# Kernel optimization log

Hardware: AMD Instinct MI355X
Metric: run time of the kernel (lower is better)

## Reference

```python
import jax, jax.numpy as jnp
import numpy as np

N, IN_DIM, OUT_DIM, HEADS, E = 50000, 256, 256, 4, 800000
HEAD_DIM = OUT_DIM // HEADS
NEG_SLOPE = 0.2


def setup_inputs() -> dict:
    key = jax.random.key(0)
    k = jax.random.split(key, 6)
    h = jax.random.normal(k[0], (N, IN_DIM), dtype=jnp.float32)
    edge_index = jax.random.randint(k[1], (2, E), 0, N, dtype=jnp.int32)
    # xavier-uniform-ish scales
    W = jax.random.normal(k[2], (OUT_DIM, IN_DIM), dtype=jnp.float32) * (1.0 / np.sqrt(IN_DIM))
    b = jnp.zeros((OUT_DIM,), dtype=jnp.float32)
    a_src = jax.random.normal(k[3], (HEADS, HEAD_DIM), dtype=jnp.float32) * (1.0 / np.sqrt(HEAD_DIM))
    a_dst = jax.random.normal(k[4], (HEADS, HEAD_DIM), dtype=jnp.float32) * (1.0 / np.sqrt(HEAD_DIM))
    return {"h": h, "edge_index": edge_index, "W": W, "b": b, "a_src": a_src, "a_dst": a_dst}


def reference(h, edge_index, W, b, a_src, a_dst):
    idx_i, idx_j = edge_index[0], edge_index[1]
    Wh = (h @ W.T + b).reshape(N, HEADS, HEAD_DIM)  # [N,H,D]
    # per-node attention logits components (avoids gathering full Wh per edge twice)
    alpha_src = jnp.einsum('nhd,hd->nh', Wh, a_src)  # [N,H]
    alpha_dst = jnp.einsum('nhd,hd->nh', Wh, a_dst)  # [N,H]
    e = jax.nn.leaky_relu(alpha_src[idx_i] + alpha_dst[idx_j], NEG_SLOPE)  # [E,H]
    # segment softmax over neighbors j of each destination row i (sparse.softmax dim=1)
    m = jax.ops.segment_max(e, idx_i, num_segments=N)  # [N,H]
    ex = jnp.exp(e - m[idx_i])
    denom = jax.ops.segment_sum(ex, idx_i, num_segments=N)  # [N,H]
    att = ex / denom[idx_i]  # [E,H]
    # sparse-mm aggregation: out_i = sum_j att_ij * Wh_j, per head
    out = jax.ops.segment_sum(att[:, :, None] * Wh[idx_j], idx_i, num_segments=N)  # [N,H,D]
    return out.reshape(N, OUT_DIM)
```

## Files before the change

### kernel.cpp

```cpp
#include <hip/hip_runtime.h>
#include <hip/hip_bf16.h>
#include <stdint.h>

constexpr int IN_DIM  = 256;
constexpr int OUT_DIM = 256;
constexpr int HEADS   = 4;
constexpr int HEAD_DIM = 64;
constexpr float NEG_SLOPE = 0.2f;

typedef __attribute__((ext_vector_type(8))) short bf16x8;
typedef __attribute__((ext_vector_type(4))) float f32x4;

static __device__ __forceinline__ unsigned short f2bf(float f) {
  union { float f; uint32_t u; } v; v.f = f;
  uint32_t u = v.u;
  return (unsigned short)((u + 0x7fffu + ((u >> 16) & 1u)) >> 16);
}

__global__ __launch_bounds__(256) void k_prep(
    const float* __restrict__ W, const float* __restrict__ b,
    const float* __restrict__ a_src, const float* __restrict__ a_dst,
    float* __restrict__ csrc, unsigned short* __restrict__ Wb) {
  int bid = blockIdx.x, t = threadIdx.x;
  if (bid < 32) {
    int base = bid * 2048 + t * 8;
    float4 f0 = *(const float4*)(W + base);
    float4 f1 = *(const float4*)(W + base + 4);
    union { unsigned short us[8]; uint4 u4; } pk;
    pk.us[0]=f2bf(f0.x); pk.us[1]=f2bf(f0.y); pk.us[2]=f2bf(f0.z); pk.us[3]=f2bf(f0.w);
    pk.us[4]=f2bf(f1.x); pk.us[5]=f2bf(f1.y); pk.us[6]=f2bf(f1.z); pk.us[7]=f2bf(f1.w);
    *(uint4*)(Wb + base) = pk.u4;
  } else if (t < 8) {
    int hh = t & 3;
    const float* a = (t < 4 ? a_src : a_dst) + hh * HEAD_DIM;
    float cs = 0.f;
    for (int d = 0; d < HEAD_DIM; ++d) cs += b[hh * HEAD_DIM + d] * a[d];
    csrc[t] = cs;
  }
}

__global__ __launch_bounds__(256) void k_gemm_mfma(
    const float* __restrict__ h, const unsigned short* __restrict__ Wb,
    const float* __restrict__ b,
    const float* __restrict__ a_src, const float* __restrict__ a_dst,
    const float* __restrict__ csrc,
    unsigned short* __restrict__ Wh,
    float* __restrict__ asrc, float* __restrict__ adst,
    const int* __restrict__ idx_i, int* __restrict__ counts, int N, int E) {
  __shared__ unsigned short lds[20480];
  const int t = threadIdx.x;
  const int w = t >> 6, l = t & 63;
  const int lm = l & 15, g = l >> 4;
  const int r0 = blockIdx.x * 64;

  f32x4 acc[4][4];
  const f32x4 fz = {0.f, 0.f, 0.f, 0.f};
#pragma unroll
  for (int fm = 0; fm < 4; ++fm)
#pragma unroll
    for (int fn = 0; fn < 4; ++fn) acc[fm][fn] = fz;

  float breg[4], asg[4], adg[4];
#pragma unroll
  for (int fn = 0; fn < 4; ++fn) {
    breg[fn] = b[w * 64 + fn * 16 + lm];
    asg[fn]  = a_src[w * 64 + fn * 16 + lm];
    adg[fn]  = a_dst[w * 64 + fn * 16 + lm];
  }

  auto stageA = [&](int ch) {
    int k0 = ch * 64;
    int row = t >> 2;
    int grow = r0 + row;
    unsigned short* dstbase = lds + row * 64;
#pragma unroll
    for (int cc = 0; cc < 2; ++cc) {
      int c = (t & 3) * 2 + cc;
      union { unsigned short us[8]; bf16x8 v; } pk;
      if (grow < N) {
        const float* src = h + (size_t)grow * 256 + k0 + c * 8;
        float4 f0 = *(const float4*)(src);
        float4 f1 = *(const float4*)(src + 4);
        pk.us[0]=f2bf(f0.x); pk.us[1]=f2bf(f0.y); pk.us[2]=f2bf(f0.z); pk.us[3]=f2bf(f0.w);
        pk.us[4]=f2bf(f1.x); pk.us[5]=f2bf(f1.y); pk.us[6]=f2bf(f1.z); pk.us[7]=f2bf(f1.w);
      } else {
#pragma unroll
        for (int e = 0; e < 8; ++e) pk.us[e] = 0;
      }
      *(bf16x8*)(dstbase + ((c ^ (row & 7)) * 8)) = pk.v;
    }
  };

  auto stageB = [&](int ch) {
    int k0 = ch * 64;
    unsigned short* Bbase = lds + 4096;
    int c  = l & 7;
    int rs = l >> 3;
#pragma unroll
    for (int i = 0; i < 8; ++i) {
      int row = w * 64 + i * 8 + rs;
      bf16x8 v = *(const bf16x8*)(Wb + (size_t)row * 256 + k0 + c * 8);
      *(bf16x8*)(Bbase + row * 64 + ((c ^ rs) * 8)) = v;
    }
  };

  auto compute = [&]() {
    const unsigned short* A = lds;
    const unsigned short* B = lds + 4096;
#pragma unroll
    for (int ks = 0; ks < 2; ++ks) {
      bf16x8 af[4], bfr[4];
#pragma unroll
      for (int fm = 0; fm < 4; ++fm) {
        int row = fm * 16 + lm;
        af[fm] = *(const bf16x8*)(A + row * 64 + (((ks * 4 + g) ^ (row & 7)) * 8));
      }
#pragma unroll
      for (int fn = 0; fn < 4; ++fn) {
        int row = w * 64 + fn * 16 + lm;
        bfr[fn] = *(const bf16x8*)(B + row * 64 + (((ks * 4 + g) ^ (row & 7)) * 8));
      }
#pragma unroll
      for (int fm = 0; fm < 4; ++fm)
#pragma unroll
        for (int fn = 0; fn < 4; ++fn)
          acc[fm][fn] = __builtin_amdgcn_mfma_f32_16x16x32_bf16(
              af[fm], bfr[fn], acc[fm][fn], 0, 0, 0);
    }
  };

#pragma unroll
  for (int ch = 0; ch < 4; ++ch) {
    stageA(ch); stageB(ch);
    __syncthreads();
    compute();
    __syncthreads();
  }

#pragma unroll
  for (int fm = 0; fm < 4; ++fm) {
#pragma unroll
    for (int r = 0; r < 4; ++r) {
      int grow = r0 + fm * 16 + g * 4 + r;
      if (grow < N) {
        size_t rowoff = (size_t)grow * 256;
#pragma unroll
        for (int fn = 0; fn < 4; ++fn) {
          int col = w * 64 + fn * 16 + lm;
          Wh[rowoff + col] = f2bf(acc[fm][fn][r] + breg[fn]);
        }
      }
    }
  }

  float cs = csrc[w], cd = csrc[4 + w];
#pragma unroll
  for (int fm = 0; fm < 4; ++fm) {
#pragma unroll
    for (int r = 0; r < 4; ++r) {
      float ps = acc[fm][0][r] * asg[0] + acc[fm][1][r] * asg[1]
               + acc[fm][2][r] * asg[2] + acc[fm][3][r] * asg[3];
      float pd = acc[fm][0][r] * adg[0] + acc[fm][1][r] * adg[1]
               + acc[fm][2][r] * adg[2] + acc[fm][3][r] * adg[3];
#pragma unroll
      for (int off = 1; off < 16; off <<= 1) {
        ps += __shfl_xor(ps, off, 64);
        pd += __shfl_xor(pd, off, 64);
      }
      if (lm == 0) {
        int grow = r0 + fm * 16 + g * 4 + r;
        if (grow < N) {
          asrc[grow * 4 + w] = ps + cs;
          adst[grow * 4 + w] = pd + cd;
        }
      }
    }
  }

  {
    long long nb = gridDim.x;
    long long e0 = (long long)blockIdx.x * E / nb;
    long long e1 = ((long long)blockIdx.x + 1) * E / nb;
    for (long long e = e0 + t; e < e1; e += 256)
      atomicAdd(&counts[idx_i[e]], 1);
  }
}

__global__ __launch_bounds__(256) void k_scanA(const int* __restrict__ counts,
                                               int* __restrict__ offsets,
                                               int* __restrict__ bsum, int N) {
  __shared__ int s[256];
  int t = threadIdx.x;
  int idx = blockIdx.x * 256 + t;
  int v = (idx < N) ? counts[idx] : 0;
  s[t] = v;
  __syncthreads();
  for (int off = 1; off < 256; off <<= 1) {
    int x = (t >= off) ? s[t - off] : 0;
    __syncthreads();
    s[t] += x;
    __syncthreads();
  }
  if (idx < N) offsets[idx] = s[t] - v;
  if (t == 255) bsum[blockIdx.x] = s[255];
}

__global__ __launch_bounds__(256) void k_scanBC(int* __restrict__ offsets,
                                                const int* __restrict__ bsum,
                                                int nb, int N) {
  __shared__ int s[256];
  int t = threadIdx.x;
  int v = (t < nb) ? bsum[t] : 0;
  s[t] = v;
  __syncthreads();
  for (int off = 1; off < 256; off <<= 1) {
    int x = (t >= off) ? s[t - off] : 0;
    __syncthreads();
    s[t] += x;
    __syncthreads();
  }
  int bid = blockIdx.x;
  int add = (bid > 0) ? s[bid - 1] : 0;
  int idx = bid * 256 + t;
  if (idx < N) offsets[idx] += add;
}

__global__ __launch_bounds__(256) void k_scatter(const int* __restrict__ idx_i,
                                                 const int* __restrict__ idx_j,
                                                 int* __restrict__ offsets,
                                                 int* __restrict__ csr_j, int E) {
  int e = blockIdx.x * 256 + threadIdx.x;
  if (e < E) {
    int i = idx_i[e];
    int p = atomicAdd(&offsets[i], 1);
    csr_j[p] = idx_j[e];
  }
}

__global__ __launch_bounds__(256) void k_aggregate(const int* __restrict__ offsets,
                                                   const int* __restrict__ csr_j,
                                                   const float* __restrict__ asrc,
                                                   const float* __restrict__ adst,
                                                   const unsigned short* __restrict__ Wh,
                                                   float* __restrict__ out, int N) {
  int t = threadIdx.x;
  int wv = t >> 6, l = t & 63;
  int half = l >> 5, ll = l & 31;
  int i = blockIdx.x * 8 + wv * 2 + half;
  bool valid = i < N;
  int beg = (valid && i > 0) ? offsets[i - 1] : 0;
  int end = valid ? offsets[i] : 0;
  int deg = end - beg;
  int hh = ll >> 3;
  float aih = valid ? asrc[i * 4 + hh] : 0.f;

  float o[8];
#pragma unroll
  for (int d = 0; d < 8; ++d) o[d] = 0.f;
  float denom = 0.f;

  for (int q = 0; q < deg; q += 8) {
    int jj[8];
    float wgt[8];
    uint4 vv[8];
#pragma unroll
    for (int k = 0; k < 8; ++k) {
      int qk = q + k;
      int qc = qk < deg - 1 ? qk : deg - 1;
      jj[k] = csr_j[beg + qc];
    }
#pragma unroll
    for (int k = 0; k < 8; ++k) {
      float s = aih + adst[(size_t)jj[k] * 4 + hh];
      s = s > 0.f ? s : NEG_SLOPE * s;
      s = (q + k < deg) ? s : -1e38f;
      wgt[k] = __expf(s);
      vv[k] = *(const uint4*)(Wh + (size_t)jj[k] * 256 + ll * 8);
    }
    denom += ((wgt[0] + wgt[1]) + (wgt[2] + wgt[3])) +
             ((wgt[4] + wgt[5]) + (wgt[6] + wgt[7]));
#pragma unroll
    for (int k = 0; k < 8; ++k) {
      union { uint32_t u; float f; } c0, c1, c2, c3, c4, c5, c6, c7;
      c0.u = vv[k].x << 16; c1.u = vv[k].x & 0xffff0000u;
      c2.u = vv[k].y << 16; c3.u = vv[k].y & 0xffff0000u;
      c4.u = vv[k].z << 16; c5.u = vv[k].z & 0xffff0000u;
      c6.u = vv[k].w << 16; c7.u = vv[k].w & 0xffff0000u;
      float wk = wgt[k];
      o[0] += wk * c0.f; o[1] += wk * c1.f;
      o[2] += wk * c2.f; o[3] += wk * c3.f;
      o[4] += wk * c4.f; o[5] += wk * c5.f;
      o[6] += wk * c6.f; o[7] += wk * c7.f;
    }
  }

  if (valid) {
    float inv = (deg > 0) ? 1.f / denom : 0.f;
    f32x4 o0 = {o[0] * inv, o[1] * inv, o[2] * inv, o[3] * inv};
    f32x4 o1 = {o[4] * inv, o[5] * inv, o[6] * inv, o[7] * inv};
    f32x4* dst = (f32x4*)(out + (size_t)i * 256 + ll * 8);
    __builtin_nontemporal_store(o0, dst);
    __builtin_nontemporal_store(o1, dst + 1);
  }
}

extern "C" void kernel_launch(void* const* d_in, const int* in_sizes, int n_in,
                              void* d_out, int out_size, void* d_ws, size_t ws_size,
                              hipStream_t stream) {
  const float* h     = (const float*)d_in[0];
  const int*   eidx  = (const int*)  d_in[1];
  const float* W     = (const float*)d_in[2];
  const float* b     = (const float*)d_in[3];
  const float* a_src = (const float*)d_in[4];
  const float* a_dst = (const float*)d_in[5];
  float* out = (float*)d_out;

  const int N = in_sizes[0] / IN_DIM;
  const int E = in_sizes[1] / 2;
  const int* idx_i = eidx;
  const int* idx_j = eidx + E;

  char* p = (char*)d_ws;
  auto alloc = [&](size_t bytes) {
    char* r = p;
    p += (bytes + 255) & ~(size_t)255;
    return r;
  };
  float* csrc = (float*)alloc(8 * sizeof(float));
  unsigned short* Wb = (unsigned short*)alloc((size_t)OUT_DIM * IN_DIM * sizeof(unsigned short));
  unsigned short* Wh = (unsigned short*)alloc((size_t)N * OUT_DIM * sizeof(unsigned short));
  float* asrc = (float*)alloc((size_t)N * HEADS * sizeof(float));
  float* adst = (float*)alloc((size_t)N * HEADS * sizeof(float));
  int* counts  = (int*)alloc((size_t)N * sizeof(int));
  int* offsets = (int*)alloc(((size_t)N + 1) * sizeof(int));
  int* bsum    = (int*)alloc(256 * sizeof(int));
  int* csrj    = (int*)alloc((size_t)E * sizeof(int));

  const int nbN = (N + 255) / 256;
  const int nbE = (E + 255) / 256;
  const int nbM = (N + 63) / 64;

  (void)hipMemsetAsync(counts, 0, (size_t)N * sizeof(int), stream);
  k_prep<<<33, 256, 0, stream>>>(W, b, a_src, a_dst, csrc, Wb);
  k_gemm_mfma<<<nbM, 256, 0, stream>>>(h, Wb, b, a_src, a_dst, csrc,
                                       Wh, asrc, adst, idx_i, counts, N, E);
  k_scanA<<<nbN, 256, 0, stream>>>(counts, offsets, bsum, N);
  k_scanBC<<<nbN, 256, 0, stream>>>(offsets, bsum, nbN, N);
  k_scatter<<<nbE, 256, 0, stream>>>(idx_i, idx_j, offsets, csrj, E);
  k_aggregate<<<(N + 7) / 8, 256, 0, stream>>>(offsets, csrj, asrc, adst, Wh, out, N);
}
```

Measured before the change: 187.8 us.

## Load GEMM operands directly to registers, fold memset into prep, widen scan

The GEMM drops LDS staging and loads h (fp32) and bf16 W fragments from global memory straight into registers. It converts them with v_cvt_pk_bf16_f32 and double-buffers the register loads across eight k-steps, with no barriers. The counts memset is folded into k_prep, saving one launch. The scan kernels now process four elements per thread, cutting the block count. Global loads become uncoalesced per-lane row reads, and the same operands are re-read by multiple waves, relying on cache instead of LDS reuse.

```diff
diff --git a/kernel.cpp b/kernel.cpp
--- a/kernel.cpp
+++ b/kernel.cpp
@@ -17,11 +17,20 @@
   return (unsigned short)((u + 0x7fffu + ((u >> 16) & 1u)) >> 16);
 }
 
+static __device__ __forceinline__ uint32_t cvt_pk(float lo, float hi) {
+  uint32_t r;
+  asm("v_cvt_pk_bf16_f32 %0, %1, %2" : "=v"(r) : "v"(lo), "v"(hi));
+  return r;
+}
+
 __global__ __launch_bounds__(256) void k_prep(
     const float* __restrict__ W, const float* __restrict__ b,
     const float* __restrict__ a_src, const float* __restrict__ a_dst,
-    float* __restrict__ csrc, unsigned short* __restrict__ Wb) {
+    float* __restrict__ csrc, unsigned short* __restrict__ Wb,
+    int* __restrict__ counts, int N) {
   int bid = blockIdx.x, t = threadIdx.x;
+  int i = bid * 256 + t;
+  if (i < N) counts[i] = 0;
   if (bid < 32) {
     int base = bid * 2048 + t * 8;
     float4 f0 = *(const float4*)(W + base);
@@ -30,7 +39,7 @@
     pk.us[0]=f2bf(f0.x); pk.us[1]=f2bf(f0.y); pk.us[2]=f2bf(f0.z); pk.us[3]=f2bf(f0.w);
     pk.us[4]=f2bf(f1.x); pk.us[5]=f2bf(f1.y); pk.us[6]=f2bf(f1.z); pk.us[7]=f2bf(f1.w);
     *(uint4*)(Wb + base) = pk.u4;
-  } else if (t < 8) {
+  } else if (bid == 32 && t < 8) {
     int hh = t & 3;
     const float* a = (t < 4 ? a_src : a_dst) + hh * HEAD_DIM;
     float cs = 0.f;
@@ -47,12 +56,21 @@
     unsigned short* __restrict__ Wh,
     float* __restrict__ asrc, float* __restrict__ adst,
     const int* __restrict__ idx_i, int* __restrict__ counts, int N, int E) {
-  __shared__ unsigned short lds[20480];
   const int t = threadIdx.x;
   const int w = t >> 6, l = t & 63;
   const int lm = l & 15, g = l >> 4;
   const int r0 = blockIdx.x * 64;
 
+  const float* aptr[4];
+  const unsigned short* bptr[4];
+#pragma unroll
+  for (int f = 0; f < 4; ++f) {
+    int grow = r0 + f * 16 + lm;
+    if (grow > N - 1) grow = N - 1;
+    aptr[f] = h + (size_t)grow * 256 + g * 8;
+    bptr[f] = Wb + (size_t)(w * 64 + f * 16 + lm) * 256 + g * 8;
+  }
+
   f32x4 acc[4][4];
   const f32x4 fz = {0.f, 0.f, 0.f, 0.f};
 #pragma unroll
@@ -68,73 +86,45 @@
     adg[fn]  = a_dst[w * 64 + fn * 16 + lm];
   }
 
-  auto stageA = [&](int ch) {
-    int k0 = ch * 64;
-    int row = t >> 2;
-    int grow = r0 + row;
-    unsigned short* dstbase = lds + row * 64;
-#pragma unroll
-    for (int cc = 0; cc < 2; ++cc) {
-      int c = (t & 3) * 2 + cc;
-      union { unsigned short us[8]; bf16x8 v; } pk;
-      if (grow < N) {
-        const float* src = h + (size_t)grow * 256 + k0 + c * 8;
-        float4 f0 = *(const float4*)(src);
-        float4 f1 = *(const float4*)(src + 4);
-        pk.us[0]=f2bf(f0.x); pk.us[1]=f2bf(f0.y); pk.us[2]=f2bf(f0.z); pk.us[3]=f2bf(f0.w);
-        pk.us[4]=f2bf(f1.x); pk.us[5]=f2bf(f1.y); pk.us[6]=f2bf(f1.z); pk.us[7]=f2bf(f1.w);
-      } else {
-#pragma unroll
-        for (int e = 0; e < 8; ++e) pk.us[e] = 0;
-      }
-      *(bf16x8*)(dstbase + ((c ^ (row & 7)) * 8)) = pk.v;
+  f32x4 aA[4][2], aB[4][2];
+  bf16x8 bA[4], bB[4];
+
+  auto load_step = [&](int s, f32x4 (&A)[4][2], bf16x8 (&B)[4]) {
+    int off = s * 32;
+#pragma unroll
+    for (int f = 0; f < 4; ++f) {
+      A[f][0] = *(const f32x4*)(aptr[f] + off);
+      A[f][1] = *(const f32x4*)(aptr[f] + off + 4);
+      B[f] = *(const bf16x8*)(bptr[f] + off);
     }
   };
 
-  auto stageB = [&](int ch) {
-    int k0 = ch * 64;
-    unsigned short* Bbase = lds + 4096;
-    int c  = l & 7;
-    int rs = l >> 3;
-#pragma unroll
-    for (int i = 0; i < 8; ++i) {
-      int row = w * 64 + i * 8 + rs;
-      bf16x8 v = *(const bf16x8*)(Wb + (size_t)row * 256 + k0 + c * 8);
-      *(bf16x8*)(Bbase + row * 64 + ((c ^ rs) * 8)) = v;
-    }
+  auto compute_step = [&](f32x4 (&A)[4][2], bf16x8 (&B)[4]) {
+    bf16x8 af[4];
+#pragma unroll
+    for (int f = 0; f < 4; ++f) {
+      union { uint32_t u[4]; bf16x8 v; } pk;
+      pk.u[0] = cvt_pk(A[f][0].x, A[f][0].y);
+      pk.u[1] = cvt_pk(A[f][0].z, A[f][0].w);
+      pk.u[2] = cvt_pk(A[f][1].x, A[f][1].y);
+      pk.u[3] = cvt_pk(A[f][1].z, A[f][1].w);
+      af[f] = pk.v;
+    }
+#pragma unroll
+    for (int fm = 0; fm < 4; ++fm)
+#pragma unroll
+      for (int fn = 0; fn < 4; ++fn)
+        acc[fm][fn] = __builtin_amdgcn_mfma_f32_16x16x32_bf16(
+            af[fm], B[fn], acc[fm][fn], 0, 0, 0);
   };
 
-  auto compute = [&]() {
-    const unsigned short* A = lds;
-    const unsigned short* B = lds + 4096;
-#pragma unroll
-    for (int ks = 0; ks < 2; ++ks) {
-      bf16x8 af[4], bfr[4];
-#pragma unroll
-      for (int fm = 0; fm < 4; ++fm) {
-        int row = fm * 16 + lm;
-        af[fm] = *(const bf16x8*)(A + row * 64 + (((ks * 4 + g) ^ (row & 7)) * 8));
-      }
-#pragma unroll
-      for (int fn = 0; fn < 4; ++fn) {
-        int row = w * 64 + fn * 16 + lm;
-        bfr[fn] = *(const bf16x8*)(B + row * 64 + (((ks * 4 + g) ^ (row & 7)) * 8));
-      }
-#pragma unroll
-      for (int fm = 0; fm < 4; ++fm)
-#pragma unroll
-        for (int fn = 0; fn < 4; ++fn)
-          acc[fm][fn] = __builtin_amdgcn_mfma_f32_16x16x32_bf16(
-              af[fm], bfr[fn], acc[fm][fn], 0, 0, 0);
-    }
-  };
-
-#pragma unroll
-  for (int ch = 0; ch < 4; ++ch) {
-    stageA(ch); stageB(ch);
-    __syncthreads();
-    compute();
-    __syncthreads();
+  load_step(0, aA, bA);
+#pragma unroll
+  for (int ss = 0; ss < 4; ++ss) {
+    if (ss * 2 + 1 < 8) load_step(ss * 2 + 1, aB, bB);
+    compute_step(aA, bA);
+    if (ss * 2 + 2 < 8) load_step(ss * 2 + 2, aA, bA);
+    compute_step(aB, bB);
   }
 
 #pragma unroll
@@ -191,9 +181,14 @@
                                                int* __restrict__ bsum, int N) {
   __shared__ int s[256];
   int t = threadIdx.x;
-  int idx = blockIdx.x * 256 + t;
-  int v = (idx < N) ? counts[idx] : 0;
-  s[t] = v;
+  int base = blockIdx.x * 1024 + t * 4;
+  int v[4], sum = 0;
+#pragma unroll
+  for (int k = 0; k < 4; ++k) {
+    v[k] = (base + k < N) ? counts[base + k] : 0;
+    sum += v[k];
+  }
+  s[t] = sum;
   __syncthreads();
   for (int off = 1; off < 256; off <<= 1) {
     int x = (t >= off) ? s[t - off] : 0;
@@ -201,7 +196,12 @@
     s[t] += x;
     __syncthreads();
   }
-  if (idx < N) offsets[idx] = s[t] - v;
+  int pre = s[t] - sum;
+#pragma unroll
+  for (int k = 0; k < 4; ++k) {
+    if (base + k < N) offsets[base + k] = pre;
+    pre += v[k];
+  }
   if (t == 255) bsum[blockIdx.x] = s[255];
 }
 
@@ -221,8 +221,10 @@
   }
   int bid = blockIdx.x;
   int add = (bid > 0) ? s[bid - 1] : 0;
-  int idx = bid * 256 + t;
-  if (idx < N) offsets[idx] += add;
+  int base = bid * 1024 + t * 4;
+#pragma unroll
+  for (int k = 0; k < 4; ++k)
+    if (base + k < N) offsets[base + k] += add;
 }
 
 __global__ __launch_bounds__(256) void k_scatter(const int* __restrict__ idx_i,
@@ -339,13 +341,13 @@
   const int nbN = (N + 255) / 256;
   const int nbE = (E + 255) / 256;
   const int nbM = (N + 63) / 64;
-
-  (void)hipMemsetAsync(counts, 0, (size_t)N * sizeof(int), stream);
-  k_prep<<<33, 256, 0, stream>>>(W, b, a_src, a_dst, csrc, Wb);
+  const int nbS = (N + 1023) / 1024;
+
+  k_prep<<<nbN, 256, 0, stream>>>(W, b, a_src, a_dst, csrc, Wb, counts, N);
   k_gemm_mfma<<<nbM, 256, 0, stream>>>(h, Wb, b, a_src, a_dst, csrc,
                                        Wh, asrc, adst, idx_i, counts, N, E);
-  k_scanA<<<nbN, 256, 0, stream>>>(counts, offsets, bsum, N);
-  k_scanBC<<<nbN, 256, 0, stream>>>(offsets, bsum, nbN, N);
+  k_scanA<<<nbS, 256, 0, stream>>>(counts, offsets, bsum, N);
+  k_scanBC<<<nbS, 256, 0, stream>>>(offsets, bsum, nbS, N);
   k_scatter<<<nbE, 256, 0, stream>>>(idx_i, idx_j, offsets, csrj, E);
   k_aggregate<<<(N + 7) / 8, 256, 0, stream>>>(offsets, csrj, asrc, adst, Wh, out, N);
 }
```

Measured after the change: 201.6 us. +7.3%, slower.

## Prefetch GEMM A tiles, split histogram out, fold memset, widen scan

Applied to the files above, without the earlier changes.

The GEMM now prefetches the next h chunk into registers while the current chunk is computed, so global load latency overlaps MFMA work. Out-of-range rows are clamped instead of branched on. The edge-count histogram moves from the GEMM tail into its own fully parallel kernel. The counts memset is folded into k_prep, and the scan kernels process 4 elements per thread so fewer blocks are needed. This adds a kernel launch and more registers in the GEMM in exchange for less serialization.

```diff
diff --git a/kernel.cpp b/kernel.cpp
--- a/kernel.cpp
+++ b/kernel.cpp
@@ -20,8 +20,11 @@
 __global__ __launch_bounds__(256) void k_prep(
     const float* __restrict__ W, const float* __restrict__ b,
     const float* __restrict__ a_src, const float* __restrict__ a_dst,
-    float* __restrict__ csrc, unsigned short* __restrict__ Wb) {
+    float* __restrict__ csrc, unsigned short* __restrict__ Wb,
+    int* __restrict__ counts, int N) {
   int bid = blockIdx.x, t = threadIdx.x;
+  int i = bid * 256 + t;
+  if (i < N) counts[i] = 0;
   if (bid < 32) {
     int base = bid * 2048 + t * 8;
     float4 f0 = *(const float4*)(W + base);
@@ -30,7 +33,7 @@
     pk.us[0]=f2bf(f0.x); pk.us[1]=f2bf(f0.y); pk.us[2]=f2bf(f0.z); pk.us[3]=f2bf(f0.w);
     pk.us[4]=f2bf(f1.x); pk.us[5]=f2bf(f1.y); pk.us[6]=f2bf(f1.z); pk.us[7]=f2bf(f1.w);
     *(uint4*)(Wb + base) = pk.u4;
-  } else if (t < 8) {
+  } else if (bid == 32 && t < 8) {
     int hh = t & 3;
     const float* a = (t < 4 ? a_src : a_dst) + hh * HEAD_DIM;
     float cs = 0.f;
@@ -45,14 +48,19 @@
     const float* __restrict__ a_src, const float* __restrict__ a_dst,
     const float* __restrict__ csrc,
     unsigned short* __restrict__ Wh,
-    float* __restrict__ asrc, float* __restrict__ adst,
-    const int* __restrict__ idx_i, int* __restrict__ counts, int N, int E) {
+    float* __restrict__ asrc, float* __restrict__ adst, int N) {
   __shared__ unsigned short lds[20480];
   const int t = threadIdx.x;
   const int w = t >> 6, l = t & 63;
   const int lm = l & 15, g = l >> 4;
   const int r0 = blockIdx.x * 64;
 
+  const int arow = t >> 2;
+  {
+  }
+  int growA = r0 + arow; if (growA > N - 1) growA = N - 1;
+  const float* aptr = h + (size_t)growA * 256;
+
   f32x4 acc[4][4];
   const f32x4 fz = {0.f, 0.f, 0.f, 0.f};
 #pragma unroll
@@ -68,26 +76,28 @@
     adg[fn]  = a_dst[w * 64 + fn * 16 + lm];
   }
 
-  auto stageA = [&](int ch) {
+  f32x4 apre[4];
+
+  auto loadA = [&](int ch) {
     int k0 = ch * 64;
-    int row = t >> 2;
-    int grow = r0 + row;
-    unsigned short* dstbase = lds + row * 64;
+#pragma unroll
+    for (int cc = 0; cc < 2; ++cc) {
+      int c = (t & 3) * 2 + cc;
+      apre[cc * 2 + 0] = *(const f32x4*)(aptr + k0 + c * 8);
+      apre[cc * 2 + 1] = *(const f32x4*)(aptr + k0 + c * 8 + 4);
+    }
+  };
+
+  auto writeA = [&]() {
+    unsigned short* dstbase = lds + arow * 64;
 #pragma unroll
     for (int cc = 0; cc < 2; ++cc) {
       int c = (t & 3) * 2 + cc;
       union { unsigned short us[8]; bf16x8 v; } pk;
-      if (grow < N) {
-        const float* src = h + (size_t)grow * 256 + k0 + c * 8;
-        float4 f0 = *(const float4*)(src);
-        float4 f1 = *(const float4*)(src + 4);
-        pk.us[0]=f2bf(f0.x); pk.us[1]=f2bf(f0.y); pk.us[2]=f2bf(f0.z); pk.us[3]=f2bf(f0.w);
-        pk.us[4]=f2bf(f1.x); pk.us[5]=f2bf(f1.y); pk.us[6]=f2bf(f1.z); pk.us[7]=f2bf(f1.w);
-      } else {
-#pragma unroll
-        for (int e = 0; e < 8; ++e) pk.us[e] = 0;
-      }
-      *(bf16x8*)(dstbase + ((c ^ (row & 7)) * 8)) = pk.v;
+      f32x4 f0 = apre[cc * 2 + 0], f1 = apre[cc * 2 + 1];
+      pk.us[0]=f2bf(f0.x); pk.us[1]=f2bf(f0.y); pk.us[2]=f2bf(f0.z); pk.us[3]=f2bf(f0.w);
+      pk.us[4]=f2bf(f1.x); pk.us[5]=f2bf(f1.y); pk.us[6]=f2bf(f1.z); pk.us[7]=f2bf(f1.w);
+      *(bf16x8*)(dstbase + ((c ^ (arow & 7)) * 8)) = pk.v;
     }
   };
 
@@ -129,12 +139,18 @@
     }
   };
 
+  loadA(0); writeA(); stageB(0);
+  __syncthreads();
 #pragma unroll
   for (int ch = 0; ch < 4; ++ch) {
-    stageA(ch); stageB(ch);
-    __syncthreads();
+    if (ch < 3) loadA(ch + 1);
     compute();
     __syncthreads();
+    if (ch < 3) {
+      writeA();
+      stageB(ch + 1);
+      __syncthreads();
+    }
   }
 
 #pragma unroll
@@ -176,14 +192,12 @@
       }
     }
   }
-
-  {
-    long long nb = gridDim.x;
-    long long e0 = (long long)blockIdx.x * E / nb;
-    long long e1 = ((long long)blockIdx.x + 1) * E / nb;
-    for (long long e = e0 + t; e < e1; e += 256)
-      atomicAdd(&counts[idx_i[e]], 1);
-  }
+}
+
+__global__ __launch_bounds__(256) void k_hist(const int* __restrict__ idx_i,
+                                              int* __restrict__ counts, int E) {
+  int e = blockIdx.x * 256 + threadIdx.x;
+  if (e < E) atomicAdd(&counts[idx_i[e]], 1);
 }
 
 __global__ __launch_bounds__(256) void k_scanA(const int* __restrict__ counts,
@@ -191,9 +205,14 @@
                                                int* __restrict__ bsum, int N) {
   __shared__ int s[256];
   int t = threadIdx.x;
-  int idx = blockIdx.x * 256 + t;
-  int v = (idx < N) ? counts[idx] : 0;
-  s[t] = v;
+  int base = blockIdx.x * 1024 + t * 4;
+  int v[4], sum = 0;
+#pragma unroll
+  for (int k = 0; k < 4; ++k) {
+    v[k] = (base + k < N) ? counts[base + k] : 0;
+    sum += v[k];
+  }
+  s[t] = sum;
   __syncthreads();
   for (int off = 1; off < 256; off <<= 1) {
     int x = (t >= off) ? s[t - off] : 0;
@@ -201,7 +220,12 @@
     s[t] += x;
     __syncthreads();
   }
-  if (idx < N) offsets[idx] = s[t] - v;
+  int pre = s[t] - sum;
+#pragma unroll
+  for (int k = 0; k < 4; ++k) {
+    if (base + k < N) offsets[base + k] = pre;
+    pre += v[k];
+  }
   if (t == 255) bsum[blockIdx.x] = s[255];
 }
 
@@ -221,8 +245,10 @@
   }
   int bid = blockIdx.x;
   int add = (bid > 0) ? s[bid - 1] : 0;
-  int idx = bid * 256 + t;
-  if (idx < N) offsets[idx] += add;
+  int base = bid * 1024 + t * 4;
+#pragma unroll
+  for (int k = 0; k < 4; ++k)
+    if (base + k < N) offsets[base + k] += add;
 }
 
 __global__ __launch_bounds__(256) void k_scatter(const int* __restrict__ idx_i,
@@ -339,13 +365,14 @@
   const int nbN = (N + 255) / 256;
   const int nbE = (E + 255) / 256;
   const int nbM = (N + 63) / 64;
-
-  (void)hipMemsetAsync(counts, 0, (size_t)N * sizeof(int), stream);
-  k_prep<<<33, 256, 0, stream>>>(W, b, a_src, a_dst, csrc, Wb);
+  const int nbS = (N + 1023) / 1024;
+
+  k_prep<<<nbN, 256, 0, stream>>>(W, b, a_src, a_dst, csrc, Wb, counts, N);
   k_gemm_mfma<<<nbM, 256, 0, stream>>>(h, Wb, b, a_src, a_dst, csrc,
-                                       Wh, asrc, adst, idx_i, counts, N, E);
-  k_scanA<<<nbN, 256, 0, stream>>>(counts, offsets, bsum, N);
-  k_scanBC<<<nbN, 256, 0, stream>>>(offsets, bsum, nbN, N);
+                                       Wh, asrc, adst, N);
+  k_hist<<<nbE, 256, 0, stream>>>(idx_i, counts, E);
+  k_scanA<<<nbS, 256, 0, stream>>>(counts, offsets, bsum, N);
+  k_scanBC<<<nbS, 256, 0, stream>>>(offsets, bsum, nbS, N);
   k_scatter<<<nbE, 256, 0, stream>>>(idx_i, idx_j, offsets, csrj, E);
   k_aggregate<<<(N + 7) / 8, 256, 0, stream>>>(offsets, csrj, asrc, adst, Wh, out, N);
 }
```

New measurement: 206.1 us. +9.7%, slower.
